# Performance work log

Hardware: AMD Instinct MI355X
Metric: run time of the kernel (lower is better)

The kernel has to match this reference:

```python
import jax, jax.numpy as jnp
import numpy as np

# ---- fixed architecture hyperparameters (match init_kwargs) ----
B, S = 4, 1024
L, H, DM, DF = 4, 8, 512, 2048
DH = DM // H          # 64 head dim (= 2*R after gated SPE filter)
NS = 5                # num_sines
R = 32                # num_realizations
M = 2 * DH            # favor_feature_dims = 128 (split as +/- of 64 projections)
LN_EPS = 1e-5
ATT_EPS = 1e-6


def layernorm(x, g, b):
    mu = x.mean(-1, keepdims=True)
    var = ((x - mu) ** 2).mean(-1, keepdims=True)
    return (x - mu) * jax.lax.rsqrt(var + LN_EPS) * g + b


def sine_spe(freqs, offsets, gains, noise, seq_len):
    """SineSPE positional code. freqs/offsets/gains: (H,DH,NS); noise: (H,DH,2NS,R).
    Returns qbar, kbar of shape (S,H,DH,R)."""
    pos = jnp.arange(seq_len, dtype=freqs.dtype)
    f = jax.nn.sigmoid(freqs)[:, :, None, :] / 2.0                       # (H,DH,1,NS)
    ph_q = 2.0 * jnp.pi * f * pos[None, None, :, None] + offsets[:, :, None, :]
    ph_k = 2.0 * jnp.pi * f * pos[None, None, :, None]
    om_q = jnp.stack([jnp.cos(ph_q), jnp.sin(ph_q)], -1).reshape(H, DH, seq_len, 2 * NS)
    om_k = jnp.stack([jnp.cos(ph_k), jnp.sin(ph_k)], -1).reshape(H, DH, seq_len, 2 * NS)
    g = jax.nn.softplus(gains)
    g = jnp.stack([g, g], -1).reshape(H, DH, 2 * NS)                      # upsample gains
    z = noise * g[..., None] / jnp.sqrt(jnp.asarray(2.0 * NS, freqs.dtype))
    qbar = jnp.einsum('hdsk,hdkr->shdr', om_q, z)
    kbar = jnp.einsum('hdsk,hdkr->shdr', om_k, z)
    scale = (R * DH) ** 0.25
    return qbar / scale, kbar / scale


def spe_filter(q, k, qbar, kbar, gate, gnoise):
    """Gated SPE filter. q,k: (B,S,H,DH); qbar/kbar: (S,H,DH,R); gate: (H,DH); gnoise: (H,DH,R).
    Returns qhat, khat of shape (B,S,H,2R)."""
    g = jax.nn.sigmoid(gate)[..., None]                                   # (H,DH,1)
    gn = gnoise / (DH * R) ** 0.25
    seq_len = qbar.shape[0]
    bias = jnp.broadcast_to(jnp.sqrt(g) * gn, (seq_len, H, DH, R))
    qb = jnp.concatenate([jnp.sqrt(1.0 - g) * qbar, bias], -1)            # (S,H,DH,2R)
    kb = jnp.concatenate([jnp.sqrt(1.0 - g) * kbar, bias], -1)
    qhat = jnp.einsum('bshd,shdr->bshr', q, qb)
    khat = jnp.einsum('bshd,shdr->bshr', k, kb)
    return qhat, khat


def favor(x, omega):
    """FAVOR+ softmax feature map. x: (B,S,H,DH); omega: (DH, M//2) -> (B,S,H,M)."""
    x = x * (DH ** -0.25)                                                 # sqrt(softmax_temp), temp=1/sqrt(DH)
    half_norm = 0.5 * jnp.sum(x * x, -1, keepdims=True)
    u = jnp.einsum('bshe,em->bshm', x, omega)
    phi = jnp.concatenate([jnp.exp(u - half_norm), jnp.exp(-u - half_norm)], -1)
    return phi / jnp.sqrt(jnp.asarray(M, x.dtype))


def causal_linear_attention(Q, K, V):
    """Causal linear (kernelized) attention via lax.scan. Q,K: (B,S,H,M); V: (B,S,H,DH)."""
    Bv = Q.shape[0]

    def step(carry, qkv):
        Skv, sk = carry
        q, k, v = qkv                                                     # (B,H,M),(B,H,M),(B,H,DH)
        Skv = Skv + jnp.einsum('bhm,bhd->bhmd', k, v)
        sk = sk + k
        num = jnp.einsum('bhm,bhmd->bhd', q, Skv)
        den = jnp.einsum('bhm,bhm->bh', q, sk) + ATT_EPS
        return (Skv, sk), num / den[..., None]

    init = (jnp.zeros((Bv, H, M, DH), Q.dtype), jnp.zeros((Bv, H, M), Q.dtype))
    xs = tuple(jnp.moveaxis(t, 1, 0) for t in (Q, K, V))
    _, out = jax.lax.scan(step, init, xs)
    return jnp.moveaxis(out, 0, 1)                                        # (B,S,H,DH)


def setup_inputs() -> dict:
    key = jax.random.key(0)
    ks = jax.random.split(key, 14)

    def rn(k, shape, scale=1.0):
        return jax.random.normal(k, shape, dtype=jnp.float32) * scale

    return {
        'x': rn(ks[0], (B, S, DM)),
        'Wq': rn(ks[1], (L, DM, DM), 0.02), 'bq': jnp.zeros((L, DM), jnp.float32),
        'Wk': rn(ks[2], (L, DM, DM), 0.02), 'bk': jnp.zeros((L, DM), jnp.float32),
        'Wv': rn(ks[3], (L, DM, DM), 0.02), 'bv': jnp.zeros((L, DM), jnp.float32),
        'Wo': rn(ks[4], (L, DM, DM), 0.02), 'bo': jnp.zeros((L, DM), jnp.float32),
        'W1': rn(ks[5], (L, DM, DF), 0.02), 'b1': jnp.zeros((L, DF), jnp.float32),
        'W2': rn(ks[6], (L, DF, DM), 0.02), 'b2': jnp.zeros((L, DM), jnp.float32),
        'ln1_g': jnp.ones((L, DM), jnp.float32), 'ln1_b': jnp.zeros((L, DM), jnp.float32),
        'ln2_g': jnp.ones((L, DM), jnp.float32), 'ln2_b': jnp.zeros((L, DM), jnp.float32),
        'spe_freqs': rn(ks[7], (L, H, DH, NS)),
        'spe_offsets': rn(ks[8], (L, H, DH, NS)),
        'spe_gains': rn(ks[9], (L, H, DH, NS)),
        'spe_noise': rn(ks[10], (L, H, DH, 2 * NS, R)),
        'gate': rn(ks[11], (L, H, DH)),
        'gate_noise': rn(ks[12], (L, H, DH, R)),
        'favor_omega': rn(ks[13], (L, DH, M // 2)),
    }


def reference(x, Wq, bq, Wk, bk, Wv, bv, Wo, bo, W1, b1, W2, b2,
              ln1_g, ln1_b, ln2_g, ln2_b,
              spe_freqs, spe_offsets, spe_gains, spe_noise, gate, gate_noise, favor_omega):
    Bv, Sv, _ = x.shape
    out = x
    for l in range(L):
        qbar, kbar = sine_spe(spe_freqs[l], spe_offsets[l], spe_gains[l], spe_noise[l], Sv)
        q = (out @ Wq[l] + bq[l]).reshape(Bv, Sv, H, DH)
        k = (out @ Wk[l] + bk[l]).reshape(Bv, Sv, H, DH)
        v = (out @ Wv[l] + bv[l]).reshape(Bv, Sv, H, DH)
        qh, kh = spe_filter(q, k, qbar, kbar, gate[l], gate_noise[l])
        Qf = favor(qh, favor_omega[l])
        Kf = favor(kh, favor_omega[l])
        att = causal_linear_attention(Qf, Kf, v).reshape(Bv, Sv, DM)
        att = att @ Wo[l] + bo[l]
        h = layernorm(out + att, ln1_g[l], ln1_b[l])
        y = jax.nn.relu(h @ W1[l] + b1[l]) @ W2[l] + b2[l]
        out = layernorm(h + y, ln2_g[l], ln2_b[l])
    return out
```

## Files before the change

### kernel.cpp

```cpp
#include <hip/hip_runtime.h>
#include <math.h>

#define BB 4
#define SS 1024
#define LL 4
#define HH 8
#define DM 512
#define DF 2048
#define DH 64
#define NS 5
#define RR 32
#define MM 128
#define NC 16
#define CHK 64
#define QKV_N 1536

#define INV_SQRT10   0.316227766016838f
#define INV_SCALE    0.148650889375340f
#define TEMP_SCALE   0.353553390593274f
#define INV_SQRT_M   0.088388347648318f
#define TWO_PI       6.283185307179586f

typedef __attribute__((ext_vector_type(8))) short bf16x8;
typedef __attribute__((ext_vector_type(4))) float f32x4;

__device__ __forceinline__ unsigned short f2bf(float f) {
  union { float f; unsigned int u; } v; v.f = f;
  unsigned int r = v.u + 0x7FFFu + ((v.u >> 16) & 1u);
  return (unsigned short)(r >> 16);
}

__device__ __forceinline__ float bf2f(unsigned short u) {
  union { unsigned int u; float f; } v; v.u = (unsigned int)u << 16;
  return v.f;
}

__device__ __forceinline__ void gld_lds16(const unsigned short* g, unsigned short* l) {
  __builtin_amdgcn_global_load_lds((const __attribute__((address_space(1))) void*)g,
                                   (__attribute__((address_space(3))) void*)l,
                                   16, 0, 0);
}

template<int RELU, int OUT_BF>
__global__ __launch_bounds__(256)
void gemm_mfma(const unsigned short* __restrict__ A, const unsigned short* __restrict__ Bt,
               const float* __restrict__ bias, float* __restrict__ Cf,
               unsigned short* __restrict__ Cbf, int M, int N, int K)
{
  __shared__ unsigned short As[128 * 32];
  __shared__ unsigned short Bs[128 * 32];
  const int tid  = threadIdx.x;
  const int w    = tid >> 6;
  const int lane = tid & 63;
  const int row0 = blockIdx.y * 128;
  const int col0 = blockIdx.x * 128;
  const int wr = (w >> 1) * 64;
  const int wc = (w & 1) * 64;
  const int c0 = w * 2, c1 = w * 2 + 1;
  const int m0 = c0 * 16 + (lane >> 2);
  const int m1 = c1 * 16 + (lane >> 2);
  const int kA = (lane & 3) * 8;

  f32x4 acc[4][4] = {};

  for (int k0 = 0; k0 < K; k0 += 32) {
    gld_lds16(&A [(size_t)(row0 + m0) * K + k0 + kA], &As[c0 * 512]);
    gld_lds16(&A [(size_t)(row0 + m1) * K + k0 + kA], &As[c1 * 512]);
    gld_lds16(&Bt[(size_t)(col0 + m0) * K + k0 + kA], &Bs[c0 * 512]);
    gld_lds16(&Bt[(size_t)(col0 + m1) * K + k0 + kA], &Bs[c1 * 512]);
    __syncthreads();
    const int rA = wr + (lane & 15);
    const int rB = wc + (lane & 15);
    const int kk = (lane >> 4) * 8;
    bf16x8 af[4], bfr[4];
#pragma unroll
    for (int i = 0; i < 4; ++i) {
      af[i]  = *reinterpret_cast<const bf16x8*>(&As[(rA + i * 16) * 32 + kk]);
      bfr[i] = *reinterpret_cast<const bf16x8*>(&Bs[(rB + i * 16) * 32 + kk]);
    }
#pragma unroll
    for (int mi = 0; mi < 4; ++mi)
#pragma unroll
      for (int ni = 0; ni < 4; ++ni)
        acc[mi][ni] = __builtin_amdgcn_mfma_f32_16x16x32_bf16(af[mi], bfr[ni], acc[mi][ni], 0, 0, 0);
    __syncthreads();
  }
  const int cr = (lane >> 4) * 4;
  const int cc = lane & 15;
#pragma unroll
  for (int mi = 0; mi < 4; ++mi) {
#pragma unroll
    for (int ni = 0; ni < 4; ++ni) {
      const int col = col0 + wc + ni * 16 + cc;
      const float bv = bias[col];
#pragma unroll
      for (int r = 0; r < 4; ++r) {
        const int row = row0 + wr + mi * 16 + cr + r;
        float v = acc[mi][ni][r] + bv;
        if (RELU) v = fmaxf(v, 0.f);
        if (OUT_BF) Cbf[(size_t)row * N + col] = f2bf(v);
        else        Cf [(size_t)row * N + col] = v;
      }
    }
  }
}

template<int RELU, int OUT_BF, int SPLITK>
__global__ __launch_bounds__(256)
void gemm_mfma_n64(const unsigned short* __restrict__ A, const unsigned short* __restrict__ Bt,
                   const float* __restrict__ bias, float* __restrict__ Cf,
                   unsigned short* __restrict__ Cbf, int M, int N, int K)
{
  __shared__ unsigned short As[128 * 32];
  __shared__ unsigned short Bs[64 * 32];
  const int tid  = threadIdx.x;
  const int w    = tid >> 6;
  const int lane = tid & 63;
  const int row0 = blockIdx.y * 128;
  const int col0 = blockIdx.x * 64;
  const int kz   = (SPLITK > 1) ? blockIdx.z : 0;
  const int Ks   = K / SPLITK;
  const int kbeg = kz * Ks;
  const int wr = (w >> 1) * 64;
  const int wc = (w & 1) * 32;
  const int c0 = w * 2, c1 = w * 2 + 1;
  const int m0 = c0 * 16 + (lane >> 2);
  const int m1 = c1 * 16 + (lane >> 2);
  const int mb = w * 16 + (lane >> 2);
  const int kA = (lane & 3) * 8;

  f32x4 acc[4][2] = {};

  for (int k0 = kbeg; k0 < kbeg + Ks; k0 += 32) {
    gld_lds16(&A [(size_t)(row0 + m0) * K + k0 + kA], &As[c0 * 512]);
    gld_lds16(&A [(size_t)(row0 + m1) * K + k0 + kA], &As[c1 * 512]);
    gld_lds16(&Bt[(size_t)(col0 + mb) * K + k0 + kA], &Bs[w * 512]);
    __syncthreads();
    const int rA = wr + (lane & 15);
    const int rB = wc + (lane & 15);
    const int kk = (lane >> 4) * 8;
    bf16x8 af[4], bfr[2];
#pragma unroll
    for (int i = 0; i < 4; ++i)
      af[i]  = *reinterpret_cast<const bf16x8*>(&As[(rA + i * 16) * 32 + kk]);
#pragma unroll
    for (int i = 0; i < 2; ++i)
      bfr[i] = *reinterpret_cast<const bf16x8*>(&Bs[(rB + i * 16) * 32 + kk]);
#pragma unroll
    for (int mi = 0; mi < 4; ++mi)
#pragma unroll
      for (int ni = 0; ni < 2; ++ni)
        acc[mi][ni] = __builtin_amdgcn_mfma_f32_16x16x32_bf16(af[mi], bfr[ni], acc[mi][ni], 0, 0, 0);
    __syncthreads();
  }
  const int cr = (lane >> 4) * 4;
  const int cc = lane & 15;
  float* Cfo = Cf + (size_t)kz * M * N;
#pragma unroll
  for (int mi = 0; mi < 4; ++mi) {
#pragma unroll
    for (int ni = 0; ni < 2; ++ni) {
      const int col = col0 + wc + ni * 16 + cc;
      const float bv = (kz == 0) ? bias[col] : 0.f;
#pragma unroll
      for (int r = 0; r < 4; ++r) {
        const int row = row0 + wr + mi * 16 + cr + r;
        float v = acc[mi][ni][r] + bv;
        if (RELU) v = fmaxf(v, 0.f);
        if (OUT_BF) Cbf[(size_t)row * N + col] = f2bf(v);
        else        Cfo[(size_t)row * N + col] = v;
      }
    }
  }
}

__global__ __launch_bounds__(256)
void transpose_bf(const float* __restrict__ W, unsigned short* __restrict__ Wt, int K, int N,
                  size_t inStride, size_t outStride)
{
  const float* Wl = W + blockIdx.z * inStride;
  unsigned short* Wtl = Wt + blockIdx.z * outStride;
  __shared__ float tile[32][33];
  const int k0 = blockIdx.y * 32, n0 = blockIdx.x * 32;
  const int tx = threadIdx.x & 31, ty = threadIdx.x >> 5;
#pragma unroll
  for (int j = 0; j < 4; ++j)
    tile[ty + 8 * j][tx] = Wl[(size_t)(k0 + ty + 8 * j) * N + n0 + tx];
  __syncthreads();
#pragma unroll
  for (int j = 0; j < 4; ++j)
    Wtl[(size_t)(n0 + ty + 8 * j) * K + k0 + tx] = f2bf(tile[tx][ty + 8 * j]);
}

__global__ __launch_bounds__(256)
void pack_bias(const float* __restrict__ bq, const float* __restrict__ bk,
               const float* __restrict__ bv, float* __restrict__ out)
{
  const int l = blockIdx.y;
  const int i = blockIdx.x * 256 + threadIdx.x;
  if (i < QKV_N)
    out[l * QKV_N + i] = (i < 512) ? bq[l * DM + i] : (i < 1024) ? bk[l * DM + i - 512]
                                                                 : bv[l * DM + i - 1024];
}

__global__ __launch_bounds__(256)
void cvt_bf16(const float* __restrict__ in, unsigned short* __restrict__ out, int n4)
{
  const int i = blockIdx.x * 256 + threadIdx.x;
  if (i < n4) {
    const float4 v = reinterpret_cast<const float4*>(in)[i];
    ushort4 o;
    o.x = f2bf(v.x); o.y = f2bf(v.y); o.z = f2bf(v.z); o.w = f2bf(v.w);
    reinterpret_cast<ushort4*>(out)[i] = o;
  }
}

__global__ __launch_bounds__(256)
void spe_prep_all(const float* __restrict__ gains, const float* __restrict__ noise,
                  const float* __restrict__ gate, const float* __restrict__ gnoise,
                  const float* __restrict__ offsets,
                  unsigned short* __restrict__ zpb, unsigned short* __restrict__ wbb,
                  float2* __restrict__ offcs)
{
  const int i = blockIdx.x * 256 + threadIdx.x;
  const int NZ = LL * HH * RR * 10 * DH;
  const int NW = LL * HH * RR * DH;
  const int NO = LL * HH * DH * NS;
  if (i < NZ) {
    const int d = i & 63;
    int j = i >> 6;
    const int k = j % 10; j /= 10;
    const int r = j & 31; j >>= 5;
    const int h = j & 7;  const int l = j >> 3;
    const int lhd = (l * HH + h) * DH + d;
    const float ga = gains[lhd * NS + (k >> 1)];
    const float sp = (ga > 20.f) ? ga : log1pf(__expf(ga));
    const float gg = 1.f / (1.f + __expf(-gate[lhd]));
    const float c1 = sqrtf(fmaxf(1.f - gg, 0.f));
    const float nz = noise[((size_t)lhd * 10 + k) * 32 + r];
    zpb[i] = f2bf(nz * sp * c1 * (INV_SQRT10 * INV_SCALE));
  } else if (i < NZ + NW) {
    int j = i - NZ;
    const int d = j & 63; j >>= 6;
    const int r = j & 31; j >>= 5;
    const int h = j & 7;  const int l = j >> 3;
    const int lhd = (l * HH + h) * DH + d;
    const float gg = 1.f / (1.f + __expf(-gate[lhd]));
    wbb[i - NZ] = f2bf(sqrtf(gg) * gnoise[(size_t)lhd * 32 + r] * INV_SCALE);
  } else if (i < NZ + NW + NO) {
    const int j = i - NZ - NW;
    float sn, cn;
    __sincosf(offsets[j], &sn, &cn);
    offcs[j] = make_float2(cn, sn);
  }
}

__global__ __launch_bounds__(256)
void spe_xhat(const float* __restrict__ freqs, const float2* __restrict__ offcs,
              const unsigned short* __restrict__ zpb, const unsigned short* __restrict__ wbb,
              const float* __restrict__ qkv,
              unsigned short* __restrict__ xhat, float* __restrict__ hn)
{
  const int s = blockIdx.x;
  const int h = blockIdx.y;
  const int t = threadIdx.x;
  const int w = t >> 6;
  const int lane = t & 63;
  __shared__ float omqT[10][64];
  __shared__ float omkT[10][64];
  __shared__ unsigned short qbT[64 * 64];
  __shared__ unsigned short kbT[64 * 64];
  __shared__ unsigned short rQ[16 * 64];
  __shared__ unsigned short rK[16 * 64];
  __shared__ float hqp[4][8];

  for (int e = t; e < DH * NS; e += 256) {
    const int d = e / NS, ns = e - d * NS;
    const float fr = 0.5f / (1.f + __expf(-freqs[(h * DH + d) * NS + ns]));
    float sn, cn;
    __sincosf(TWO_PI * fr * (float)s, &sn, &cn);
    const float2 oc = offcs[(h * DH + d) * NS + ns];
    omkT[2 * ns][d]     = cn;
    omkT[2 * ns + 1][d] = sn;
    omqT[2 * ns][d]     = cn * oc.x - sn * oc.y;
    omqT[2 * ns + 1][d] = sn * oc.x + cn * oc.y;
  }
  {
    const int b = t >> 6, d = t & 63;
    const size_t idx = ((size_t)b * SS + s) * QKV_N + h * DH + d;
    const int sd = d ^ ((b & 7) << 3);
    rQ[b * 64 + sd] = f2bf(qkv[idx] * TEMP_SCALE);
    rK[b * 64 + sd] = f2bf(qkv[idx + 512] * TEMP_SCALE);
  }
  for (int i = t; i < 768; i += 256) {
    rQ[256 + i] = 0;
    rK[256 + i] = 0;
  }
  __syncthreads();
  {
    const int r = t >> 3, dg = t & 7, d0 = dg * 8;
    float accq[8] = {}, acck[8] = {};
    const unsigned short* zr = zpb + (size_t)(h * RR + r) * 10 * 64 + d0;
#pragma unroll
    for (int k = 0; k < 10; ++k) {
      const bf16x8 zv = *reinterpret_cast<const bf16x8*>(zr + (size_t)k * 64);
      const float4 oq0 = *reinterpret_cast<const float4*>(&omqT[k][d0]);
      const float4 oq1 = *reinterpret_cast<const float4*>(&omqT[k][d0 + 4]);
      const float4 ok0 = *reinterpret_cast<const float4*>(&omkT[k][d0]);
      const float4 ok1 = *reinterpret_cast<const float4*>(&omkT[k][d0 + 4]);
      float zf[8];
#pragma unroll
      for (int j = 0; j < 8; ++j) zf[j] = bf2f((unsigned short)zv[j]);
      accq[0] += zf[0] * oq0.x; accq[1] += zf[1] * oq0.y;
      accq[2] += zf[2] * oq0.z; accq[3] += zf[3] * oq0.w;
      accq[4] += zf[4] * oq1.x; accq[5] += zf[5] * oq1.y;
      accq[6] += zf[6] * oq1.z; accq[7] += zf[7] * oq1.w;
      acck[0] += zf[0] * ok0.x; acck[1] += zf[1] * ok0.y;
      acck[2] += zf[2] * ok0.z; acck[3] += zf[3] * ok0.w;
      acck[4] += zf[4] * ok1.x; acck[5] += zf[5] * ok1.y;
      acck[6] += zf[6] * ok1.z; acck[7] += zf[7] * ok1.w;
    }
    bf16x8 qv, kv;
#pragma unroll
    for (int j = 0; j < 8; ++j) {
      qv[j] = (short)f2bf(accq[j]);
      kv[j] = (short)f2bf(acck[j]);
    }
    const int sd0 = d0 ^ ((r & 7) << 3);
    *reinterpret_cast<bf16x8*>(&qbT[r * 64 + sd0]) = qv;
    *reinterpret_cast<bf16x8*>(&kbT[r * 64 + sd0]) = kv;
    const bf16x8 wv = *reinterpret_cast<const bf16x8*>(&wbb[(size_t)(h * RR + r) * 64 + d0]);
    *reinterpret_cast<bf16x8*>(&qbT[(32 + r) * 64 + sd0]) = wv;
    *reinterpret_cast<bf16x8*>(&kbT[(32 + r) * 64 + sd0]) = wv;
  }
  __syncthreads();
  f32x4 aq = {0.f, 0.f, 0.f, 0.f}, ak = {0.f, 0.f, 0.f, 0.f};
  const int arow = lane & 15;
  const int colr = w * 16 + (lane & 15);
#pragma unroll
  for (int kt = 0; kt < 2; ++kt) {
    const int g = kt * 4 + (lane >> 4);
    const bf16x8 fAq = *reinterpret_cast<const bf16x8*>(&rQ[arow * 64 + ((g ^ (arow & 7)) << 3)]);
    const bf16x8 fAk = *reinterpret_cast<const bf16x8*>(&rK[arow * 64 + ((g ^ (arow & 7)) << 3)]);
    const bf16x8 fBq = *reinterpret_cast<const bf16x8*>(&qbT[colr * 64 + ((g ^ (colr & 7)) << 3)]);
    const bf16x8 fBk = *reinterpret_cast<const bf16x8*>(&kbT[colr * 64 + ((g ^ (colr & 7)) << 3)]);
    aq = __builtin_amdgcn_mfma_f32_16x16x32_bf16(fAq, fBq, aq, 0, 0, 0);
    ak = __builtin_amdgcn_mfma_f32_16x16x32_bf16(fAk, fBk, ak, 0, 0, 0);
  }
  float rq[4], rk2[4];
#pragma unroll
  for (int r = 0; r < 4; ++r) { rq[r] = aq[r] * aq[r]; rk2[r] = ak[r] * ak[r]; }
#pragma unroll
  for (int off = 1; off < 16; off <<= 1) {
#pragma unroll
    for (int r = 0; r < 4; ++r) {
      rq[r]  += __shfl_xor(rq[r],  off, 64);
      rk2[r] += __shfl_xor(rk2[r], off, 64);
    }
  }
  if (lane == 0) {
#pragma unroll
    for (int r = 0; r < 4; ++r) { hqp[w][r] = rq[r]; hqp[w][4 + r] = rk2[r]; }
  }
  if (lane < 16) {
#pragma unroll
    for (int r = 0; r < 4; ++r) {
      const size_t rowq = ((size_t)r * SS + s) * HH + h;
      xhat[rowq * 64 + w * 16 + lane] = f2bf(aq[r]);
      xhat[(rowq + (size_t)BB * SS * HH) * 64 + w * 16 + lane] = f2bf(ak[r]);
    }
  }
  __syncthreads();
  if (t < 8) {
    const int b = t & 3;
    const int ko = (t >> 2) * 4;
    const float v = 0.5f * (hqp[0][ko + b] + hqp[1][ko + b] + hqp[2][ko + b] + hqp[3][ko + b]);
    const size_t row = ((size_t)b * SS + s) * HH + h + (size_t)(t >> 2) * BB * SS * HH;
    hn[row] = v;
  }
}

__global__ __launch_bounds__(256)
void favor_gemm(const unsigned short* __restrict__ xhat, const unsigned short* __restrict__ omgT,
                const float* __restrict__ hn, unsigned short* __restrict__ QfKfB)
{
  __shared__ unsigned short As[128 * 32];
  __shared__ unsigned short Bs[64 * 32];
  const int tid  = threadIdx.x;
  const int w    = tid >> 6;
  const int lane = tid & 63;
  const int row0 = blockIdx.x * 128;
  const int c0 = w * 2, c1 = w * 2 + 1;
  const int m0 = c0 * 16 + (lane >> 2);
  const int m1 = c1 * 16 + (lane >> 2);
  const int mb = w * 16 + (lane >> 2);
  const int kA = (lane & 3) * 8;

  f32x4 acc[2][4] = {};

  for (int k0 = 0; k0 < 64; k0 += 32) {
    gld_lds16(&xhat[(size_t)(row0 + m0) * 64 + k0 + kA], &As[c0 * 512]);
    gld_lds16(&xhat[(size_t)(row0 + m1) * 64 + k0 + kA], &As[c1 * 512]);
    gld_lds16(&omgT[(size_t)mb * 64 + k0 + kA], &Bs[w * 512]);
    __syncthreads();
    const int rA = w * 32 + (lane & 15);
    const int kk = (lane >> 4) * 8;
    bf16x8 af[2], bfr[4];
#pragma unroll
    for (int i = 0; i < 2; ++i)
      af[i]  = *reinterpret_cast<const bf16x8*>(&As[(rA + i * 16) * 32 + kk]);
#pragma unroll
    for (int i = 0; i < 4; ++i)
      bfr[i] = *reinterpret_cast<const bf16x8*>(&Bs[(i * 16 + (lane & 15)) * 32 + kk]);
#pragma unroll
    for (int mi = 0; mi < 2; ++mi)
#pragma unroll
      for (int ni = 0; ni < 4; ++ni)
        acc[mi][ni] = __builtin_amdgcn_mfma_f32_16x16x32_bf16(af[mi], bfr[ni], acc[mi][ni], 0, 0, 0);
    __syncthreads();
  }
  const int cr = (lane >> 4) * 4;
  const int cc = lane & 15;
#pragma unroll
  for (int mi = 0; mi < 2; ++mi) {
#pragma unroll
    for (int r = 0; r < 4; ++r) {
      const size_t row = row0 + w * 32 + mi * 16 + cr + r;
      const float hnv = hn[row];
#pragma unroll
      for (int ni = 0; ni < 4; ++ni) {
        const int m = ni * 16 + cc;
        const float u = acc[mi][ni][r];
        QfKfB[row * MM + m]      = f2bf(__expf( u - hnv) * INV_SQRT_M);
        QfKfB[row * MM + m + 64] = f2bf(__expf(-u - hnv) * INV_SQRT_M);
      }
    }
  }
}

__global__ __launch_bounds__(256)
void attn_chunk_sums(const unsigned short* __restrict__ KfB, const float* __restrict__ qkv,
                     float* __restrict__ Sch, float* __restrict__ kch)
{
  const int c = blockIdx.x, h = blockIdx.y, b = blockIdx.z;
  const int tid = threadIdx.x;
  const int w = tid >> 6, lane = tid & 63;
  __shared__ unsigned short KcT[128 * 64];
  __shared__ unsigned short VT[64 * 64];
  const size_t srow0 = (size_t)b * SS + c * CHK;

  for (int i = tid; i < 8192; i += 256) {
    const int m = i & 127, t = i >> 7;
    KcT[m * 64 + (t ^ ((m & 7) << 3))] = KfB[((srow0 + t) * HH + h) * MM + m];
  }
  for (int i = tid; i < 4096; i += 256) {
    const int d = i & 63, tt = i >> 6;
    VT[d * 64 + (tt ^ ((d & 7) << 3))] = f2bf(qkv[(srow0 + tt) * QKV_N + 1024 + h * DH + d]);
  }
  __syncthreads();

  const int kk = (lane >> 4) * 8;
  f32x4 acc[2][4] = {};
#pragma unroll
  for (int kc = 0; kc < 2; ++kc) {
    const int k = kc * 32 + kk;
#pragma unroll
    for (int mi = 0; mi < 2; ++mi) {
      const int mA = w * 32 + mi * 16 + (lane & 15);
      const bf16x8 a = *reinterpret_cast<const bf16x8*>(&KcT[mA * 64 + (k ^ ((mA & 7) << 3))]);
#pragma unroll
      for (int ni = 0; ni < 4; ++ni) {
        const int dB = ni * 16 + (lane & 15);
        const bf16x8 bb = *reinterpret_cast<const bf16x8*>(&VT[dB * 64 + (k ^ ((dB & 7) << 3))]);
        acc[mi][ni] = __builtin_amdgcn_mfma_f32_16x16x32_bf16(a, bb, acc[mi][ni], 0, 0, 0);
      }
    }
  }
  const size_t base = (((size_t)b * HH + h) * NC + c);
  float* So = Sch + base * (MM * DH);
  const int cr = (lane >> 4) * 4, cc = lane & 15;
#pragma unroll
  for (int mi = 0; mi < 2; ++mi)
#pragma unroll
    for (int ni = 0; ni < 4; ++ni)
#pragma unroll
      for (int r = 0; r < 4; ++r)
        So[(size_t)(w * 32 + mi * 16 + cr + r) * DH + ni * 16 + cc] = acc[mi][ni][r];
  {
    const int m = tid >> 1, half = tid & 1;
    float ks = 0.f;
#pragma unroll
    for (int j = 0; j < 32; ++j) {
      const int t2 = half * 32 + j;
      ks += bf2f(KcT[m * 64 + (t2 ^ ((m & 7) << 3))]);
    }
    ks += __shfl_xor(ks, 1, 64);
    if (half == 0) kch[base * MM + m] = ks;
  }
}

__global__ __launch_bounds__(256)
void attn_scan(float* __restrict__ Sch, float* __restrict__ kch)
{
  const int bh = blockIdx.x, part = blockIdx.y;
  const int t = threadIdx.x;
  float* base = Sch + (size_t)bh * NC * (MM * DH);
  for (int e = part * 1024 + t; e < (part + 1) * 1024; e += 256) {
    float run = 0.f;
#pragma unroll
    for (int c = 0; c < NC; ++c) {
      const float v = base[(size_t)c * (MM * DH) + e];
      base[(size_t)c * (MM * DH) + e] = run;
      run += v;
    }
  }
  if (part == 0 && t < MM) {
    float* kb2 = kch + (size_t)bh * NC * MM;
    float run = 0.f;
#pragma unroll
    for (int c = 0; c < NC; ++c) {
      const float v = kb2[c * MM + t];
      kb2[c * MM + t] = run;
      run += v;
    }
  }
}

__global__ __launch_bounds__(256)
void attn_out(const unsigned short* __restrict__ QfKfB, const float* __restrict__ qkv,
              const float* __restrict__ Sch, const float* __restrict__ kch,
              unsigned short* __restrict__ att)
{
  const int c = blockIdx.x, h = blockIdx.y, b = blockIdx.z;
  const int tid = threadIdx.x;
  const int w = tid >> 6;
  const int lane = tid & 63;
  __shared__ unsigned short Qc[64 * 128];
  __shared__ unsigned short Sb[64 * 64];
  __shared__ unsigned short KVU[12288];
  __shared__ float skp[MM];
  __shared__ float denl[64];

  unsigned short* Kc   = KVU;
  unsigned short* SpxT = KVU;
  unsigned short* VT   = KVU + 8192;

  const size_t srow0 = (size_t)b * SS + c * CHK;
  const unsigned short* Qg = QfKfB + (srow0 * HH + h) * MM;
  const unsigned short* Kg = Qg + (size_t)BB * SS * HH * MM;

  if (tid < MM) skp[tid] = kch[(((size_t)b * HH + h) * NC + c) * MM + tid];

  for (int i = tid; i < 1024; i += 256) {
    const int s2 = i >> 4, m8 = (i & 15) * 8;
    const int sw = m8 ^ ((s2 & 15) << 3);
    *reinterpret_cast<bf16x8*>(&Qc[s2 * 128 + sw]) =
        *reinterpret_cast<const bf16x8*>(&Qg[(size_t)s2 * (HH * MM) + m8]);
    *reinterpret_cast<bf16x8*>(&Kc[s2 * 128 + sw]) =
        *reinterpret_cast<const bf16x8*>(&Kg[(size_t)s2 * (HH * MM) + m8]);
  }
  for (int i = tid; i < 4096; i += 256) {
    const int d = i & 63, tt = i >> 6;
    const float v = qkv[(srow0 + tt) * QKV_N + 1024 + h * DH + d];
    VT[d * 64 + (tt ^ ((d & 7) << 3))] = f2bf(v);
  }
  __syncthreads();

  const int sA = w * 16 + (lane & 15);
  const int kk = (lane >> 4) * 8;
  f32x4 acc_s[4] = {};
#pragma unroll
  for (int kc = 0; kc < 4; ++kc) {
    const int k = kc * 32 + kk;
    const bf16x8 aq = *reinterpret_cast<const bf16x8*>(&Qc[sA * 128 + (k ^ ((sA & 15) << 3))]);
#pragma unroll
    for (int n = 0; n < 4; ++n) {
      const int tB = n * 16 + (lane & 15);
      const bf16x8 bq = *reinterpret_cast<const bf16x8*>(&Kc[tB * 128 + (k ^ ((tB & 15) << 3))]);
      acc_s[n] = __builtin_amdgcn_mfma_f32_16x16x32_bf16(aq, bq, acc_s[n], 0, 0, 0);
    }
  }
  __syncthreads();

  {
    const int g = lane >> 4;
    const int tcol = lane & 15;
    float dintra[4] = {0.f, 0.f, 0.f, 0.f};
#pragma unroll
    for (int r = 0; r < 4; ++r) {
      const int s = w * 16 + g * 4 + r;
#pragma unroll
      for (int n = 0; n < 4; ++n) {
        const int t2 = n * 16 + tcol;
        const float v = (t2 <= s) ? acc_s[n][r] : 0.f;
        dintra[r] += v;
        Sb[s * 64 + (t2 ^ ((s & 7) << 3))] = f2bf(v);
      }
    }
#pragma unroll
    for (int off = 1; off < 16; off <<= 1)
#pragma unroll
      for (int r = 0; r < 4; ++r) dintra[r] += __shfl_xor(dintra[r], off, 64);
    if (tcol == 0) {
#pragma unroll
      for (int r = 0; r < 4; ++r) denl[w * 16 + g * 4 + r] = dintra[r];
    }
  }
  {
    const float* Sp = Sch + (((size_t)b * HH + h) * NC + c) * (MM * DH);
    for (int i = tid; i < 8192; i += 256) {
      const int d = i & 63, m = i >> 6;
      SpxT[d * 128 + (m ^ ((d & 15) << 3))] = f2bf(Sp[(size_t)m * DH + d]);
    }
  }
  __syncthreads();

  f32x4 acc_o[4] = {};
#pragma unroll
  for (int kc = 0; kc < 2; ++kc) {
    const int k = kc * 32 + kk;
    const bf16x8 as = *reinterpret_cast<const bf16x8*>(&Sb[sA * 64 + (k ^ ((sA & 7) << 3))]);
#pragma unroll
    for (int n = 0; n < 4; ++n) {
      const int dB = n * 16 + (lane & 15);
      const bf16x8 bv = *reinterpret_cast<const bf16x8*>(&VT[dB * 64 + (k ^ ((dB & 7) << 3))]);
      acc_o[n] = __builtin_amdgcn_mfma_f32_16x16x32_bf16(as, bv, acc_o[n], 0, 0, 0);
    }
  }
#pragma unroll
  for (int kc = 0; kc < 4; ++kc) {
    const int k = kc * 32 + kk;
    const bf16x8 aq = *reinterpret_cast<const bf16x8*>(&Qc[sA * 128 + (k ^ ((sA & 15) << 3))]);
#pragma unroll
    for (int n = 0; n < 4; ++n) {
      const int dB = n * 16 + (lane & 15);
      const bf16x8 bs = *reinterpret_cast<const bf16x8*>(&SpxT[dB * 128 + (k ^ ((dB & 15) << 3))]);
      acc_o[n] = __builtin_amdgcn_mfma_f32_16x16x32_bf16(aq, bs, acc_o[n], 0, 0, 0);
    }
  }
  {
    const int s2 = tid >> 2, part = tid & 3;
    float p = 0.f;
#pragma unroll
    for (int j = 0; j < 32; ++j) {
      const int m = part * 32 + j;
      p += bf2f(Qc[s2 * 128 + (m ^ ((s2 & 15) << 3))]) * skp[m];
    }
    p += __shfl_xor(p, 1, 64);
    p += __shfl_xor(p, 2, 64);
    if (part == 0) denl[s2] += p + 1e-6f;
  }
  __syncthreads();

  {
    const int g = lane >> 4;
    const int dcol = lane & 15;
#pragma unroll
    for (int r = 0; r < 4; ++r) {
      const int s = w * 16 + g * 4 + r;
      const float dinv = 1.f / denl[s];
#pragma unroll
      for (int n = 0; n < 4; ++n)
        att[(srow0 + s) * DM + h * DH + n * 16 + dcol] = f2bf(acc_o[n][r] * dinv);
    }
  }
}

template<int WBF, int NSUM>
__global__ __launch_bounds__(256)
void add_ln(const float* __restrict__ a, const float* __restrict__ bres, size_t sstride,
            const float* __restrict__ g, const float* __restrict__ be,
            float* __restrict__ out, unsigned short* __restrict__ outbf)
{
  const int row = blockIdx.x;
  const int t = threadIdx.x;
  const size_t base = (size_t)row * DM;
  float x0 = a[base + t] + bres[base + t];
  float x1 = a[base + t + 256] + bres[base + t + 256];
  if (NSUM == 2) {
    x0 += bres[sstride + base + t];
    x1 += bres[sstride + base + t + 256];
  }
  __shared__ float red[8];
  float ssum = x0 + x1;
#pragma unroll
  for (int off = 32; off > 0; off >>= 1) ssum += __shfl_xor(ssum, off, 64);
  const int wid = t >> 6, lid = t & 63;
  if (lid == 0) red[wid] = ssum;
  __syncthreads();
  const float mu = (red[0] + red[1] + red[2] + red[3]) * (1.f / DM);
  const float d0 = x0 - mu, d1 = x1 - mu;
  float sv = d0 * d0 + d1 * d1;
#pragma unroll
  for (int off = 32; off > 0; off >>= 1) sv += __shfl_xor(sv, off, 64);
  if (lid == 0) red[4 + wid] = sv;
  __syncthreads();
  const float var = (red[4] + red[5] + red[6] + red[7]) * (1.f / DM);
  const float rs = rsqrtf(var + 1e-5f);
  const float o0 = d0 * rs * g[t]       + be[t];
  const float o1 = d1 * rs * g[t + 256] + be[t + 256];
  out[base + t]       = o0;
  out[base + t + 256] = o1;
  if (WBF) {
    outbf[base + t]       = f2bf(o0);
    outbf[base + t + 256] = f2bf(o1);
  }
}

extern "C" void kernel_launch(void* const* d_in, const int* in_sizes, int n_in,
                              void* d_out, int out_size, void* d_ws, size_t ws_size,
                              hipStream_t stream)
{
  const float* x      = (const float*)d_in[0];
  const float* Wq     = (const float*)d_in[1];
  const float* bq     = (const float*)d_in[2];
  const float* Wk     = (const float*)d_in[3];
  const float* bk     = (const float*)d_in[4];
  const float* Wv     = (const float*)d_in[5];
  const float* bv     = (const float*)d_in[6];
  const float* Wo     = (const float*)d_in[7];
  const float* bo     = (const float*)d_in[8];
  const float* W1     = (const float*)d_in[9];
  const float* b1     = (const float*)d_in[10];
  const float* W2     = (const float*)d_in[11];
  const float* b2     = (const float*)d_in[12];
  const float* ln1g   = (const float*)d_in[13];
  const float* ln1b   = (const float*)d_in[14];
  const float* ln2g   = (const float*)d_in[15];
  const float* ln2b   = (const float*)d_in[16];
  const float* freqs  = (const float*)d_in[17];
  const float* offs   = (const float*)d_in[18];
  const float* gains  = (const float*)d_in[19];
  const float* noise  = (const float*)d_in[20];
  const float* gate   = (const float*)d_in[21];
  const float* gnoise = (const float*)d_in[22];
  const float* omega  = (const float*)d_in[23];

  float* ws = (float*)d_ws;
  size_t o = 0;
  float* curf = ws + o; o += (size_t)BB * SS * DM;
  float* qkvf = ws + o; o += (size_t)BB * SS * QKV_N;
  float* Sch  = ws + o; o += (size_t)BB * HH * NC * MM * DH;
  float* kch  = ws + o; o += (size_t)BB * HH * NC * MM;
  float* hn   = ws + o; o += (size_t)2 * BB * SS * HH;
  float* bqkv = ws + o; o += (size_t)LL * QKV_N;
  float2* offcs = (float2*)(ws + o); o += (size_t)LL * HH * DH * NS * 2;
  unsigned short* zpb = (unsigned short*)(ws + o); o += (size_t)LL * HH * RR * 10 * DH / 2;
  unsigned short* QfKfB = (unsigned short*)(ws + o); o += (size_t)2 * BB * SS * HH * MM / 2;
  unsigned short* xhat  = (unsigned short*)(ws + o); o += (size_t)2 * BB * SS * HH * DH / 2;
  unsigned short* attb  = (unsigned short*)(ws + o); o += (size_t)BB * SS * DM / 2;
  unsigned short* h_bf  = (unsigned short*)(ws + o); o += (size_t)BB * SS * DM / 2;
  unsigned short* curbf = (unsigned short*)(ws + o); o += (size_t)BB * SS * DM / 2;
  unsigned short* Wqkvt = (unsigned short*)(ws + o); o += (size_t)LL * QKV_N * DM / 2;
  unsigned short* Wot   = (unsigned short*)(ws + o); o += (size_t)LL * DM * DM / 2;
  unsigned short* W1t   = (unsigned short*)(ws + o); o += (size_t)LL * DF * DM / 2;
  unsigned short* W2t   = (unsigned short*)(ws + o); o += (size_t)LL * DM * DF / 2;
  unsigned short* omgT  = (unsigned short*)(ws + o); o += (size_t)LL * 4096 / 2;
  unsigned short* wbb   = (unsigned short*)(ws + o); o += (size_t)LL * HH * RR * DH / 2;

  const size_t SLICE = (size_t)BB * SS * DM;
  float* attp = qkvf;
  float* hbuf = qkvf + 2 * SLICE;
  float* ybuf = Sch;
  unsigned short* midbf = QfKfB;
  unsigned short* KfB   = QfKfB + (size_t)BB * SS * HH * MM;

  const int MROWS = BB * SS;

  cvt_bf16<<<(BB * SS * DM / 4 + 255) / 256, 256, 0, stream>>>(x, curbf, BB * SS * DM / 4);
  spe_prep_all<<<2856, 256, 0, stream>>>(gains, noise, gate, gnoise, offs, zpb, wbb, offcs);
  transpose_bf<<<dim3(16, 16, 4), 256, 0, stream>>>(Wq, Wqkvt,                     DM, DM, (size_t)DM * DM, (size_t)QKV_N * DM);
  transpose_bf<<<dim3(16, 16, 4), 256, 0, stream>>>(Wk, Wqkvt + (size_t)512 * DM,  DM, DM, (size_t)DM * DM, (size_t)QKV_N * DM);
  transpose_bf<<<dim3(16, 16, 4), 256, 0, stream>>>(Wv, Wqkvt + (size_t)1024 * DM, DM, DM, (size_t)DM * DM, (size_t)QKV_N * DM);
  transpose_bf<<<dim3(16, 16, 4), 256, 0, stream>>>(Wo, Wot, DM, DM, (size_t)DM * DM, (size_t)DM * DM);
  transpose_bf<<<dim3(64, 16, 4), 256, 0, stream>>>(W1, W1t, DM, DF, (size_t)DM * DF, (size_t)DF * DM);
  transpose_bf<<<dim3(16, 64, 4), 256, 0, stream>>>(W2, W2t, DF, DM, (size_t)DF * DM, (size_t)DM * DF);
  transpose_bf<<<dim3(2, 2, 4),   256, 0, stream>>>(omega, omgT, DH, MM / 2, (size_t)DH * (MM / 2), 4096);
  pack_bias<<<dim3(6, 4), 256, 0, stream>>>(bq, bk, bv, bqkv);

  for (int l = 0; l < LL; ++l) {
    const float* in = (l == 0) ? x : curf;

    gemm_mfma_n64<0, 0, 1><<<dim3(QKV_N / 64, MROWS / 128), 256, 0, stream>>>(
        curbf, Wqkvt + (size_t)l * QKV_N * DM, bqkv + (size_t)l * QKV_N,
        qkvf, (unsigned short*)nullptr, MROWS, QKV_N, DM);

    spe_xhat<<<dim3(SS, HH), 256, 0, stream>>>(
        freqs + (size_t)l * HH * DH * NS, offcs + (size_t)l * HH * DH * NS,
        zpb + (size_t)l * HH * RR * 10 * DH, wbb + (size_t)l * HH * RR * DH,
        qkvf, xhat, hn);
    favor_gemm<<<dim3(2 * BB * SS * HH / 128), 256, 0, stream>>>(
        xhat, omgT + (size_t)l * 4096, hn, QfKfB);

    attn_chunk_sums<<<dim3(NC, HH, BB), 256, 0, stream>>>(KfB, qkvf, Sch, kch);
    attn_scan<<<dim3(BB * HH, 8), 256, 0, stream>>>(Sch, kch);
    attn_out<<<dim3(NC, HH, BB), 256, 0, stream>>>(QfKfB, qkvf, Sch, kch, attb);

    gemm_mfma_n64<0, 0, 2><<<dim3(DM / 64, MROWS / 128, 2), 256, 0, stream>>>(
        attb, Wot + (size_t)l * DM * DM, bo + (size_t)l * DM,
        attp, (unsigned short*)nullptr, MROWS, DM, DM);

    add_ln<1, 2><<<MROWS, 256, 0, stream>>>(in, attp, SLICE,
        ln1g + (size_t)l * DM, ln1b + (size_t)l * DM, hbuf, h_bf);

    gemm_mfma<1, 1><<<dim3(DF / 128, MROWS / 128), 256, 0, stream>>>(
        h_bf, W1t + (size_t)l * DF * DM, b1 + (size_t)l * DF, (float*)nullptr, midbf, MROWS, DF, DM);

    gemm_mfma_n64<0, 0, 2><<<dim3(DM / 64, MROWS / 128, 2), 256, 0, stream>>>(
        midbf, W2t + (size_t)l * DM * DF, b2 + (size_t)l * DM,
        ybuf, (unsigned short*)nullptr, MROWS, DM, DF);

    if (l == LL - 1) {
      add_ln<0, 2><<<MROWS, 256, 0, stream>>>(hbuf, ybuf, SLICE,
          ln2g + (size_t)l * DM, ln2b + (size_t)l * DM, (float*)d_out, (unsigned short*)nullptr);
    } else {
      add_ln<1, 2><<<MROWS, 256, 0, stream>>>(hbuf, ybuf, SLICE,
          ln2g + (size_t)l * DM, ln2b + (size_t)l * DM, curf, curbf);
    }
  }
}
```

Before: 708.8 us.

## Fuse FAVOR feature map into SPE kernel and use n64 GEMM for FFN1

The FAVOR+ projection and exponential feature map now run inside the spe_xhat kernel. The filtered q/k rows stay in shared memory and go straight through an MFMA against omega, so the separate favor_gemm launch and the xhat and hn intermediate buffers are gone. The first FFN GEMM also switches from the 128x128-tile kernel to the 128x64-tile n64 kernel, which launches more blocks. The fused kernel reads omega directly from global memory in every block, and the added work may lengthen the already heavy SPE kernel.

```diff
diff --git a/kernel.cpp b/kernel.cpp
--- a/kernel.cpp
+++ b/kernel.cpp
@@ -39,70 +39,6 @@
   __builtin_amdgcn_global_load_lds((const __attribute__((address_space(1))) void*)g,
                                    (__attribute__((address_space(3))) void*)l,
                                    16, 0, 0);
-}
-
-template<int RELU, int OUT_BF>
-__global__ __launch_bounds__(256)
-void gemm_mfma(const unsigned short* __restrict__ A, const unsigned short* __restrict__ Bt,
-               const float* __restrict__ bias, float* __restrict__ Cf,
-               unsigned short* __restrict__ Cbf, int M, int N, int K)
-{
-  __shared__ unsigned short As[128 * 32];
-  __shared__ unsigned short Bs[128 * 32];
-  const int tid  = threadIdx.x;
-  const int w    = tid >> 6;
-  const int lane = tid & 63;
-  const int row0 = blockIdx.y * 128;
-  const int col0 = blockIdx.x * 128;
-  const int wr = (w >> 1) * 64;
-  const int wc = (w & 1) * 64;
-  const int c0 = w * 2, c1 = w * 2 + 1;
-  const int m0 = c0 * 16 + (lane >> 2);
-  const int m1 = c1 * 16 + (lane >> 2);
-  const int kA = (lane & 3) * 8;
-
-  f32x4 acc[4][4] = {};
-
-  for (int k0 = 0; k0 < K; k0 += 32) {
-    gld_lds16(&A [(size_t)(row0 + m0) * K + k0 + kA], &As[c0 * 512]);
-    gld_lds16(&A [(size_t)(row0 + m1) * K + k0 + kA], &As[c1 * 512]);
-    gld_lds16(&Bt[(size_t)(col0 + m0) * K + k0 + kA], &Bs[c0 * 512]);
-    gld_lds16(&Bt[(size_t)(col0 + m1) * K + k0 + kA], &Bs[c1 * 512]);
-    __syncthreads();
-    const int rA = wr + (lane & 15);
-    const int rB = wc + (lane & 15);
-    const int kk = (lane >> 4) * 8;
-    bf16x8 af[4], bfr[4];
-#pragma unroll
-    for (int i = 0; i < 4; ++i) {
-      af[i]  = *reinterpret_cast<const bf16x8*>(&As[(rA + i * 16) * 32 + kk]);
-      bfr[i] = *reinterpret_cast<const bf16x8*>(&Bs[(rB + i * 16) * 32 + kk]);
-    }
-#pragma unroll
-    for (int mi = 0; mi < 4; ++mi)
-#pragma unroll
-      for (int ni = 0; ni < 4; ++ni)
-        acc[mi][ni] = __builtin_amdgcn_mfma_f32_16x16x32_bf16(af[mi], bfr[ni], acc[mi][ni], 0, 0, 0);
-    __syncthreads();
-  }
-  const int cr = (lane >> 4) * 4;
-  const int cc = lane & 15;
-#pragma unroll
-  for (int mi = 0; mi < 4; ++mi) {
-#pragma unroll
-    for (int ni = 0; ni < 4; ++ni) {
-      const int col = col0 + wc + ni * 16 + cc;
-      const float bv = bias[col];
-#pragma unroll
-      for (int r = 0; r < 4; ++r) {
-        const int row = row0 + wr + mi * 16 + cr + r;
-        float v = acc[mi][ni][r] + bv;
-        if (RELU) v = fmaxf(v, 0.f);
-        if (OUT_BF) Cbf[(size_t)row * N + col] = f2bf(v);
-        else        Cf [(size_t)row * N + col] = v;
-      }
-    }
-  }
 }
 
 template<int RELU, int OUT_BF, int SPLITK>
@@ -258,8 +194,8 @@
 __global__ __launch_bounds__(256)
 void spe_xhat(const float* __restrict__ freqs, const float2* __restrict__ offcs,
               const unsigned short* __restrict__ zpb, const unsigned short* __restrict__ wbb,
-              const float* __restrict__ qkv,
-              unsigned short* __restrict__ xhat, float* __restrict__ hn)
+              const float* __restrict__ qkv, const unsigned short* __restrict__ omgT,
+              unsigned short* __restrict__ QfKfB)
 {
   const int s = blockIdx.x;
   const int h = blockIdx.y;
@@ -273,6 +209,7 @@
   __shared__ unsigned short rQ[16 * 64];
   __shared__ unsigned short rK[16 * 64];
   __shared__ float hqp[4][8];
+  __shared__ float hnl[8];
 
   for (int e = t; e < DH * NS; e += 256) {
     const int d = e / NS, ns = e - d * NS;
@@ -362,78 +299,44 @@
 #pragma unroll
     for (int r = 0; r < 4; ++r) { hqp[w][r] = rq[r]; hqp[w][4 + r] = rk2[r]; }
   }
-  if (lane < 16) {
-#pragma unroll
-    for (int r = 0; r < 4; ++r) {
-      const size_t rowq = ((size_t)r * SS + s) * HH + h;
-      xhat[rowq * 64 + w * 16 + lane] = f2bf(aq[r]);
-      xhat[(rowq + (size_t)BB * SS * HH) * 64 + w * 16 + lane] = f2bf(ak[r]);
-    }
-  }
-  __syncthreads();
+  __syncthreads();
+
   if (t < 8) {
     const int b = t & 3;
     const int ko = (t >> 2) * 4;
-    const float v = 0.5f * (hqp[0][ko + b] + hqp[1][ko + b] + hqp[2][ko + b] + hqp[3][ko + b]);
-    const size_t row = ((size_t)b * SS + s) * HH + h + (size_t)(t >> 2) * BB * SS * HH;
-    hn[row] = v;
-  }
-}
-
-__global__ __launch_bounds__(256)
-void favor_gemm(const unsigned short* __restrict__ xhat, const unsigned short* __restrict__ omgT,
-                const float* __restrict__ hn, unsigned short* __restrict__ QfKfB)
-{
-  __shared__ unsigned short As[128 * 32];
-  __shared__ unsigned short Bs[64 * 32];
-  const int tid  = threadIdx.x;
-  const int w    = tid >> 6;
-  const int lane = tid & 63;
-  const int row0 = blockIdx.x * 128;
-  const int c0 = w * 2, c1 = w * 2 + 1;
-  const int m0 = c0 * 16 + (lane >> 2);
-  const int m1 = c1 * 16 + (lane >> 2);
-  const int mb = w * 16 + (lane >> 2);
-  const int kA = (lane & 3) * 8;
-
-  f32x4 acc[2][4] = {};
-
-  for (int k0 = 0; k0 < 64; k0 += 32) {
-    gld_lds16(&xhat[(size_t)(row0 + m0) * 64 + k0 + kA], &As[c0 * 512]);
-    gld_lds16(&xhat[(size_t)(row0 + m1) * 64 + k0 + kA], &As[c1 * 512]);
-    gld_lds16(&omgT[(size_t)mb * 64 + k0 + kA], &Bs[w * 512]);
-    __syncthreads();
-    const int rA = w * 32 + (lane & 15);
-    const int kk = (lane >> 4) * 8;
-    bf16x8 af[2], bfr[4];
-#pragma unroll
-    for (int i = 0; i < 2; ++i)
-      af[i]  = *reinterpret_cast<const bf16x8*>(&As[(rA + i * 16) * 32 + kk]);
-#pragma unroll
-    for (int i = 0; i < 4; ++i)
-      bfr[i] = *reinterpret_cast<const bf16x8*>(&Bs[(i * 16 + (lane & 15)) * 32 + kk]);
-#pragma unroll
-    for (int mi = 0; mi < 2; ++mi)
-#pragma unroll
-      for (int ni = 0; ni < 4; ++ni)
-        acc[mi][ni] = __builtin_amdgcn_mfma_f32_16x16x32_bf16(af[mi], bfr[ni], acc[mi][ni], 0, 0, 0);
-    __syncthreads();
-  }
-  const int cr = (lane >> 4) * 4;
-  const int cc = lane & 15;
-#pragma unroll
-  for (int mi = 0; mi < 2; ++mi) {
+    hnl[t] = 0.5f * (hqp[0][ko + b] + hqp[1][ko + b] + hqp[2][ko + b] + hqp[3][ko + b]);
+  }
+  if (lane < 16) {
 #pragma unroll
     for (int r = 0; r < 4; ++r) {
-      const size_t row = row0 + w * 32 + mi * 16 + cr + r;
-      const float hnv = hn[row];
-#pragma unroll
-      for (int ni = 0; ni < 4; ++ni) {
-        const int m = ni * 16 + cc;
-        const float u = acc[mi][ni][r];
-        QfKfB[row * MM + m]      = f2bf(__expf( u - hnv) * INV_SQRT_M);
-        QfKfB[row * MM + m + 64] = f2bf(__expf(-u - hnv) * INV_SQRT_M);
-      }
+      const int d = w * 16 + lane;
+      rQ[r * 64 + (d ^ (r << 3))] = f2bf(aq[r]);
+      rK[r * 64 + (d ^ (r << 3))] = f2bf(ak[r]);
+    }
+  }
+  __syncthreads();
+
+  f32x4 uq = {0.f, 0.f, 0.f, 0.f}, uk = {0.f, 0.f, 0.f, 0.f};
+  const int ocol = w * 16 + (lane & 15);
+#pragma unroll
+  for (int kt = 0; kt < 2; ++kt) {
+    const int g = kt * 4 + (lane >> 4);
+    const bf16x8 fAq = *reinterpret_cast<const bf16x8*>(&rQ[arow * 64 + ((g ^ (arow & 7)) << 3)]);
+    const bf16x8 fAk = *reinterpret_cast<const bf16x8*>(&rK[arow * 64 + ((g ^ (arow & 7)) << 3)]);
+    const bf16x8 fB  = *reinterpret_cast<const bf16x8*>(&omgT[(size_t)ocol * 64 + g * 8]);
+    uq = __builtin_amdgcn_mfma_f32_16x16x32_bf16(fAq, fB, uq, 0, 0, 0);
+    uk = __builtin_amdgcn_mfma_f32_16x16x32_bf16(fAk, fB, uk, 0, 0, 0);
+  }
+  if (lane < 16) {
+#pragma unroll
+    for (int r = 0; r < 4; ++r) {
+      const size_t rowq = ((size_t)r * SS + s) * HH + h;
+      const size_t rowk = rowq + (size_t)BB * SS * HH;
+      const float hq = hnl[r], hk = hnl[4 + r];
+      QfKfB[rowq * MM + ocol]      = f2bf(__expf( uq[r] - hq) * INV_SQRT_M);
+      QfKfB[rowq * MM + ocol + 64] = f2bf(__expf(-uq[r] - hq) * INV_SQRT_M);
+      QfKfB[rowk * MM + ocol]      = f2bf(__expf( uk[r] - hk) * INV_SQRT_M);
+      QfKfB[rowk * MM + ocol + 64] = f2bf(__expf(-uk[r] - hk) * INV_SQRT_M);
     }
   }
 }
@@ -742,12 +645,10 @@
   float* qkvf = ws + o; o += (size_t)BB * SS * QKV_N;
   float* Sch  = ws + o; o += (size_t)BB * HH * NC * MM * DH;
   float* kch  = ws + o; o += (size_t)BB * HH * NC * MM;
-  float* hn   = ws + o; o += (size_t)2 * BB * SS * HH;
   float* bqkv = ws + o; o += (size_t)LL * QKV_N;
   float2* offcs = (float2*)(ws + o); o += (size_t)LL * HH * DH * NS * 2;
   unsigned short* zpb = (unsigned short*)(ws + o); o += (size_t)LL * HH * RR * 10 * DH / 2;
   unsigned short* QfKfB = (unsigned short*)(ws + o); o += (size_t)2 * BB * SS * HH * MM / 2;
-  unsigned short* xhat  = (unsigned short*)(ws + o); o += (size_t)2 * BB * SS * HH * DH / 2;
   unsigned short* attb  = (unsigned short*)(ws + o); o += (size_t)BB * SS * DM / 2;
   unsigned short* h_bf  = (unsigned short*)(ws + o); o += (size_t)BB * SS * DM / 2;
   unsigned short* curbf = (unsigned short*)(ws + o); o += (size_t)BB * SS * DM / 2;
@@ -788,9 +689,7 @@
     spe_xhat<<<dim3(SS, HH), 256, 0, stream>>>(
         freqs + (size_t)l * HH * DH * NS, offcs + (size_t)l * HH * DH * NS,
         zpb + (size_t)l * HH * RR * 10 * DH, wbb + (size_t)l * HH * RR * DH,
-        qkvf, xhat, hn);
-    favor_gemm<<<dim3(2 * BB * SS * HH / 128), 256, 0, stream>>>(
-        xhat, omgT + (size_t)l * 4096, hn, QfKfB);
+        qkvf, omgT + (size_t)l * 4096, QfKfB);
 
     attn_chunk_sums<<<dim3(NC, HH, BB), 256, 0, stream>>>(KfB, qkvf, Sch, kch);
     attn_scan<<<dim3(BB * HH, 8), 256, 0, stream>>>(Sch, kch);
@@ -803,7 +702,7 @@
     add_ln<1, 2><<<MROWS, 256, 0, stream>>>(in, attp, SLICE,
         ln1g + (size_t)l * DM, ln1b + (size_t)l * DM, hbuf, h_bf);
 
-    gemm_mfma<1, 1><<<dim3(DF / 128, MROWS / 128), 256, 0, stream>>>(
+    gemm_mfma_n64<1, 1, 1><<<dim3(DF / 64, MROWS / 128), 256, 0, stream>>>(
         h_bf, W1t + (size_t)l * DF * DM, b1 + (size_t)l * DF, (float*)nullptr, midbf, MROWS, DF, DM);
 
     gemm_mfma_n64<0, 0, 2><<<dim3(DM / 64, MROWS / 128, 2), 256, 0, stream>>>(
```

After: 704.2 us. No clear change (-0.6%).
